# Optimization experiments

Measured on AMD Instinct MI355X. Metric: run time of the kernel, lower is better.

## Reference

```python
import jax, jax.numpy as jnp
import numpy as np

B, S, D, H = 2, 2048, 1024, 16
HD = D // H  # head_dim = 64
SCALE = HD ** -0.5


def setup_inputs() -> dict:
    key = jax.random.key(0)
    ks = jax.random.split(key, 5)
    s = 0.02
    return {
        "query": jax.random.normal(ks[0], (B, S, D), dtype=jnp.float32),
        "Wq": jax.random.normal(ks[1], (D, D), dtype=jnp.float32) * s,
        "bq": jnp.zeros((D,), dtype=jnp.float32),
        "Wk": jax.random.normal(ks[2], (D, D), dtype=jnp.float32) * s,
        "bk": jnp.zeros((D,), dtype=jnp.float32),
        "Wv": jax.random.normal(ks[3], (D, D), dtype=jnp.float32) * s,
        "bv": jnp.zeros((D,), dtype=jnp.float32),
        "Wo": jax.random.normal(ks[4], (D, D), dtype=jnp.float32) * s,
        "bo": jnp.zeros((D,), dtype=jnp.float32),
    }


def reference(query, Wq, bq, Wk, bk, Wv, bv, Wo, bo):
    b, s, _ = query.shape
    # QKV projections (self-attention: key = value = query)
    Q = (query @ Wq + bq).reshape(b, s, H, HD).transpose(0, 2, 1, 3)  # bhqd
    K = (query @ Wk + bk).reshape(b, s, H, HD).transpose(0, 2, 1, 3)  # bhkd
    V = (query @ Wv + bv).reshape(b, s, H, HD).transpose(0, 2, 1, 3)  # bhvd
    scores = jnp.einsum('bhqd,bhkd->bhqk', Q, K) * SCALE
    weights = jax.nn.softmax(scores, axis=-1)
    out = jnp.einsum('bhqk,bhkd->bhqd', weights, V)
    out = out.transpose(0, 2, 1, 3).reshape(b, s, D)
    return out @ Wo + bo
```

## Files before the change

kernel.cpp:

```cpp
#include <hip/hip_runtime.h>
#include <hip/hip_bf16.h>
#include <math.h>

#define B_ 2
#define S_ 2048
#define D_ 1024
#define H_ 16
#define HD_ 64
#define M_ (B_*S_)
#define C1_ 0.1803368798f

typedef float f32x4 __attribute__((ext_vector_type(4)));
typedef float f32x16 __attribute__((ext_vector_type(16)));
typedef short s16x8 __attribute__((ext_vector_type(8)));

__device__ __forceinline__ short f2bf(float f) {
  union { float f; unsigned u; } x; x.f = f;
  unsigned r = x.u + 0x7fffu + ((x.u >> 16) & 1u);
  return (short)(r >> 16);
}
__device__ __forceinline__ float bf2f(short v) {
  union { unsigned u; float f; } x; x.u = ((unsigned)(unsigned short)v) << 16;
  return x.f;
}
__device__ __forceinline__ unsigned cvt_pk_bf16(float a, float b) {
  unsigned r;
  asm("v_cvt_pk_bf16_f32 %0, %1, %2" : "=v"(r) : "v"(a), "v"(b));
  return r;
}
__device__ __forceinline__ float exp2_fast(float x) {
#if __has_builtin(__builtin_amdgcn_exp2f)
  return __builtin_amdgcn_exp2f(x);
#else
  float r; asm("v_exp_f32 %0, %1" : "=v"(r) : "v"(x)); return r;
#endif
}
__device__ __forceinline__ void gload_lds16(const void* g, void* l) {
  __builtin_amdgcn_global_load_lds(
      (const __attribute__((address_space(1))) void*)g,
      (__attribute__((address_space(3))) void*)l, 16, 0, 0);
}

__global__ __launch_bounds__(256) void k_prep(
    const float* __restrict__ query, short* __restrict__ xbf,
    const float* __restrict__ W0, const float* __restrict__ W1,
    const float* __restrict__ W2, const float* __restrict__ W3,
    short* __restrict__ T0, short* __restrict__ T1,
    short* __restrict__ T2, short* __restrict__ T3) {
  __shared__ short lt[64][72];
  const int blk = blockIdx.x;
  const int t = threadIdx.x;
  if (blk < 1024) {
    const int z = blk >> 8, tile = blk & 255;
    const float* W = z == 0 ? W0 : z == 1 ? W1 : z == 2 ? W2 : W3;
    short* Wt      = z == 0 ? T0 : z == 1 ? T1 : z == 2 ? T2 : T3;
    const int r0 = (tile >> 4) * 64;
    const int c0 = (tile & 15) * 64;
    const int rr = t >> 4, c4 = (t & 15) * 4;
    #pragma unroll
    for (int p = 0; p < 4; ++p) {
      int row = p * 16 + rr;
      f32x4 v = *reinterpret_cast<const f32x4*>(W + (size_t)(r0 + row) * D_ + c0 + c4);
      #pragma unroll
      for (int j = 0; j < 4; ++j) lt[c4 + j][row] = f2bf(v[j]);
    }
    __syncthreads();
    #pragma unroll
    for (int p = 0; p < 2; ++p) {
      int slot = p * 256 + t;
      int row = slot >> 3, s = slot & 7;
      s16x8 v = *reinterpret_cast<const s16x8*>(&lt[row][s * 8]);
      *reinterpret_cast<s16x8*>(Wt + (size_t)(c0 + row) * D_ + r0 + s * 8) = v;
    }
  } else {
    int i = ((blk - 1024) * 256 + t) * 8;
    f32x4 a = *reinterpret_cast<const f32x4*>(query + i);
    f32x4 b = *reinterpret_cast<const f32x4*>(query + i + 4);
    s16x8 v;
    v[0]=f2bf(a[0]); v[1]=f2bf(a[1]); v[2]=f2bf(a[2]); v[3]=f2bf(a[3]);
    v[4]=f2bf(b[0]); v[5]=f2bf(b[1]); v[6]=f2bf(b[2]); v[7]=f2bf(b[3]);
    *reinterpret_cast<s16x8*>(xbf + i) = v;
  }
}

__global__ __launch_bounds__(256) void k_gemm_qkv(
    const short* __restrict__ A,
    const short* __restrict__ WtQ, const short* __restrict__ WtK, const short* __restrict__ WtV,
    const float* __restrict__ bQ, const float* __restrict__ bK, const float* __restrict__ bV,
    short* __restrict__ Qo, short* __restrict__ Ko, short* __restrict__ Vto) {
  __shared__ __align__(16) char lds[65536];
  const int z = blockIdx.z;
  const short* Bt   = z == 0 ? WtQ : z == 1 ? WtK : WtV;
  const float* bias = z == 0 ? bQ  : z == 1 ? bK  : bV;
  const int t = threadIdx.x;
  const int lane = t & 63, wid = t >> 6;
  const int l15 = lane & 15, l4 = lane >> 4;
  const int wm = wid >> 1, wn = wid & 1;
  const int m0 = blockIdx.x * 128, n0 = blockIdx.y * 128;

  f32x4 acc[4][4];
  #pragma unroll
  for (int i = 0; i < 4; ++i)
    #pragma unroll
    for (int j = 0; j < 4; ++j) acc[i][j] = (f32x4){0.f, 0.f, 0.f, 0.f};

  auto stage = [&](int k0, int buf) {
    char* base = lds + buf * 32768;
    #pragma unroll
    for (int i = 0; i < 4; ++i) {
      int slot = t + i * 256;
      int row = slot >> 3, sw = (t & 7) ^ (row & 7);
      gload_lds16(A  + (size_t)(m0 + row) * D_ + k0 + sw * 8, base + (i * 256 + wid * 64) * 16);
      gload_lds16(Bt + (size_t)(n0 + row) * D_ + k0 + sw * 8, base + 16384 + (i * 256 + wid * 64) * 16);
    }
  };

  stage(0, 0);
  __syncthreads();

  int buf = 0;
  for (int k0 = 0; k0 < D_; k0 += 64, buf ^= 1) {
    if (k0 + 64 < D_) stage(k0 + 64, buf ^ 1);
    const char* bA = lds + buf * 32768;
    const char* bB = bA + 16384;
    #pragma unroll
    for (int ks = 0; ks < 2; ++ks) {
      s16x8 af[4], bf[4];
      #pragma unroll
      for (int mt = 0; mt < 4; ++mt) {
        int row = wm * 64 + mt * 16 + l15;
        af[mt] = *reinterpret_cast<const s16x8*>(bA + row * 128 + (((ks*4 + l4) ^ (row & 7)) * 16));
      }
      #pragma unroll
      for (int nt = 0; nt < 4; ++nt) {
        int row = wn * 64 + nt * 16 + l15;
        bf[nt] = *reinterpret_cast<const s16x8*>(bB + row * 128 + (((ks*4 + l4) ^ (row & 7)) * 16));
      }
      #pragma unroll
      for (int mt = 0; mt < 4; ++mt)
        #pragma unroll
        for (int nt = 0; nt < 4; ++nt)
          acc[mt][nt] = __builtin_amdgcn_mfma_f32_16x16x32_bf16(af[mt], bf[nt], acc[mt][nt], 0, 0, 0);
    }
    __syncthreads();
  }

  const float scale = (z == 0) ? C1_ : 1.f;
  #pragma unroll
  for (int nt = 0; nt < 4; ++nt) {
    int cl = wn * 64 + nt * 16 + l15;
    float bv = bias[n0 + cl];
    #pragma unroll
    for (int mt = 0; mt < 4; ++mt) {
      #pragma unroll
      for (int r = 0; r < 4; ++r) {
        int rl = wm * 64 + mt * 16 + l4 * 4 + r;
        short hv = f2bf((acc[mt][nt][r] + bv) * scale);
        if (z == 2) *reinterpret_cast<short*>(lds + cl * 256 + rl * 2) = hv;
        else        *reinterpret_cast<short*>(lds + rl * 256 + cl * 2) = hv;
      }
    }
  }
  __syncthreads();
  short* outp = (z == 0) ? Qo : (z == 1) ? Ko : Vto;
  const size_t ld   = (z == 2) ? (size_t)M_ : (size_t)D_;
  const int rowbase = (z == 2) ? n0 : m0;
  const int colbase = (z == 2) ? m0 : n0;
  #pragma unroll
  for (int p = 0; p < 8; ++p) {
    int slot = p * 256 + t;
    int row = slot >> 4, s = slot & 15;
    s16x8 v = *reinterpret_cast<const s16x8*>(lds + row * 256 + s * 16);
    *reinterpret_cast<s16x8*>(outp + (size_t)(rowbase + row) * ld + colbase + s * 8) = v;
  }
}

__global__ __launch_bounds__(256) void k_gemm_out(const short* __restrict__ A,
                                                  const short* __restrict__ Bt,
                                                  const float* __restrict__ bias,
                                                  float* __restrict__ C) {
  __shared__ __align__(16) char lds[49152];
  const int t = threadIdx.x;
  const int lane = t & 63, wid = t >> 6;
  const int l15 = lane & 15, l4 = lane >> 4;
  const int wm = wid >> 1, wn = wid & 1;
  const int m0 = blockIdx.x * 128, n0 = blockIdx.y * 64;

  f32x4 acc[4][2];
  #pragma unroll
  for (int i = 0; i < 4; ++i)
    #pragma unroll
    for (int j = 0; j < 2; ++j) acc[i][j] = (f32x4){0.f, 0.f, 0.f, 0.f};

  auto stage = [&](int k0, int buf) {
    char* base = lds + buf * 24576;
    #pragma unroll
    for (int i = 0; i < 4; ++i) {
      int slot = t + i * 256;
      int row = slot >> 3, sw = (t & 7) ^ (row & 7);
      gload_lds16(A + (size_t)(m0 + row) * D_ + k0 + sw * 8, base + (i * 256 + wid * 64) * 16);
    }
    #pragma unroll
    for (int i = 0; i < 2; ++i) {
      int slot = t + i * 256;
      int row = slot >> 3, sw = (t & 7) ^ (row & 7);
      gload_lds16(Bt + (size_t)(n0 + row) * D_ + k0 + sw * 8,
                  base + 16384 + (i * 256 + wid * 64) * 16);
    }
  };

  stage(0, 0);
  __syncthreads();

  int buf = 0;
  for (int k0 = 0; k0 < D_; k0 += 64, buf ^= 1) {
    if (k0 + 64 < D_) stage(k0 + 64, buf ^ 1);
    const char* bA = lds + buf * 24576;
    const char* bB = bA + 16384;
    #pragma unroll
    for (int ks = 0; ks < 2; ++ks) {
      s16x8 af[4], bf[2];
      #pragma unroll
      for (int mt = 0; mt < 4; ++mt) {
        int row = wm * 64 + mt * 16 + l15;
        af[mt] = *reinterpret_cast<const s16x8*>(bA + row * 128 + (((ks*4 + l4) ^ (row & 7)) * 16));
      }
      #pragma unroll
      for (int nt = 0; nt < 2; ++nt) {
        int row = wn * 32 + nt * 16 + l15;
        bf[nt] = *reinterpret_cast<const s16x8*>(bB + row * 128 + (((ks*4 + l4) ^ (row & 7)) * 16));
      }
      #pragma unroll
      for (int mt = 0; mt < 4; ++mt)
        #pragma unroll
        for (int nt = 0; nt < 2; ++nt)
          acc[mt][nt] = __builtin_amdgcn_mfma_f32_16x16x32_bf16(af[mt], bf[nt], acc[mt][nt], 0, 0, 0);
    }
    __syncthreads();
  }
  #pragma unroll
  for (int nt = 0; nt < 2; ++nt) {
    int col = n0 + wn * 32 + nt * 16 + l15;
    float bv = bias[col];
    #pragma unroll
    for (int mt = 0; mt < 4; ++mt) {
      int row0 = m0 + wm * 64 + mt * 16 + l4 * 4;
      #pragma unroll
      for (int r = 0; r < 4; ++r)
        C[(size_t)(row0 + r) * D_ + col] = acc[mt][nt][r] + bv;
    }
  }
}

__global__ __launch_bounds__(256, 4) void k_attn(const short* __restrict__ Q,
                                                 const short* __restrict__ K,
                                                 const short* __restrict__ Vt,
                                                 short* __restrict__ U0,
                                                 short* __restrict__ U1,
                                                 float* __restrict__ lsum) {
  __shared__ __align__(16) char lds[32768];
  const int t = threadIdx.x;
  const int lane = t & 63, wid = t >> 6;
  const int l31 = lane & 31, hi = lane >> 5;
  const int orig = blockIdx.x;
  const int xcd = orig & 7, idx = orig >> 3;
  const int bh = xcd * 4 + (idx >> 5);
  const int rem = idx & 31;
  const int qblk = rem >> 1;
  const int half = rem & 1;
  const int b = bh >> 4, h = bh & 15;
  const int q0 = qblk * 128;
  const size_t qkbase = (size_t)b * S_ * D_ + h * HD_;
  const short* gK = K + qkbase + (size_t)(half * (S_ / 2)) * D_;
  const short* gVt = Vt + (size_t)(h * HD_) * M_ + (size_t)b * S_ + half * (S_ / 2);
  short* Up = half ? U1 : U0;

  s16x8 qf[4];
  {
    const short* qp = Q + qkbase + (size_t)(q0 + wid * 32 + l31) * D_ + hi * 8;
    qf[0] = *reinterpret_cast<const s16x8*>(qp);
    qf[1] = *reinterpret_cast<const s16x8*>(qp + 16);
    qf[2] = *reinterpret_cast<const s16x8*>(qp + 32);
    qf[3] = *reinterpret_cast<const s16x8*>(qp + 48);
  }

  f32x16 oa[2];
  #pragma unroll
  for (int i = 0; i < 16; ++i) { oa[0][i] = 0.f; oa[1][i] = 0.f; }
  float l_run = 0.f;

  const int tr3 = t >> 3;
  const int ssw8 = ((t & 7) ^ (tr3 & 7)) * 8;
  const size_t kSrc = (size_t)tr3 * D_ + ssw8;
  const size_t vSrc = (size_t)tr3 * M_ + ssw8;

  const int s7 = l31 & 7;
  const int rbase = l31 * 128;
  int soff[4];
  #pragma unroll
  for (int ks = 0; ks < 4; ++ks) soff[ks] = ((2 * ks + hi) ^ s7) * 16;

  auto stage = [&](int tl, int bb) {
    if (tl >= S_ / 128) return;
    const short* pk = gK + (size_t)(tl * 64) * D_ + kSrc;
    const short* pv = gVt + tl * 64 + vSrc;
    char* dK = lds + bb * 8192 + wid * 1024;
    char* dV = dK + 16384;
    gload_lds16(pk, dK);
    gload_lds16(pk + (size_t)32 * D_, dK + 4096);
    gload_lds16(pv, dV);
    gload_lds16(pv + (size_t)32 * M_, dV + 4096);
  };

  auto tileFn = [&](int bb, int tl) {
    stage(tl + 1, bb ^ 1);
    const char* bK = lds + bb * 8192;
    const char* bV = bK + 16384;

    f32x16 sc[2];
    #pragma unroll
    for (int i = 0; i < 16; ++i) { sc[0][i] = 0.f; sc[1][i] = 0.f; }
    __builtin_amdgcn_s_setprio(1);
    #pragma unroll
    for (int ks = 0; ks < 4; ++ks)
      #pragma unroll
      for (int blk = 0; blk < 2; ++blk) {
        s16x8 kf = *reinterpret_cast<const s16x8*>(bK + blk * 4096 + rbase + soff[ks]);
        sc[blk] = __builtin_amdgcn_mfma_f32_32x32x16_bf16(kf, qf[ks], sc[blk], 0, 0, 0);
      }
    __builtin_amdgcn_s_setprio(0);

    float rs = 0.f;
    unsigned pkA[2][4], pkB[2][4];
    #pragma unroll
    for (int blk = 0; blk < 2; ++blk)
      #pragma unroll
      for (int g = 0; g < 4; ++g) {
        float p0 = exp2_fast(sc[blk][4*g+0]), p1 = exp2_fast(sc[blk][4*g+1]);
        float p2 = exp2_fast(sc[blk][4*g+2]), p3 = exp2_fast(sc[blk][4*g+3]);
        rs += (p0 + p1) + (p2 + p3);
        pkA[blk][g] = cvt_pk_bf16(p0, p1);
        pkB[blk][g] = cvt_pk_bf16(p2, p3);
      }
    rs += __shfl_xor(rs, 32);
    l_run += rs;

    __builtin_amdgcn_s_setprio(1);
    #pragma unroll
    for (int sp = 0; sp < 4; ++sp) {
      const int blk = sp >> 1, su = sp & 1;
      unsigned a0 = pkA[blk][2*su],     a1 = pkB[blk][2*su];
      unsigned b0 = pkA[blk][2*su + 1], b1 = pkB[blk][2*su + 1];
      asm("v_permlane32_swap_b32 %0, %1" : "+v"(a0), "+v"(b0));
      asm("v_permlane32_swap_b32 %0, %1" : "+v"(a1), "+v"(b1));
      union { unsigned u[4]; s16x8 v; } pw;
      pw.u[0] = a0; pw.u[1] = a1; pw.u[2] = b0; pw.u[3] = b1;
      #pragma unroll
      for (int dblk = 0; dblk < 2; ++dblk) {
        s16x8 vf = *reinterpret_cast<const s16x8*>(bV + dblk * 4096 + rbase + soff[sp]);
        oa[dblk] = __builtin_amdgcn_mfma_f32_32x32x16_bf16(pw.v, vf, oa[dblk], 0, 0, 0);
      }
    }
    __builtin_amdgcn_s_setprio(0);
    __syncthreads();
  };

  stage(0, 0);
  __syncthreads();
  #pragma unroll 1
  for (int it = 0; it < S_ / 256; ++it) {
    tileFn(0, 2 * it);
    tileFn(1, 2 * it + 1);
  }

  char* myl = lds + wid * 4096;
  #pragma unroll
  for (int reg = 0; reg < 16; ++reg) {
    int qrow = (reg & 3) + 8 * (reg >> 2) + 4 * hi;
    *reinterpret_cast<short*>(myl + qrow * 128 + l31 * 2)        = f2bf(oa[0][reg]);
    *reinterpret_cast<short*>(myl + qrow * 128 + (32 + l31) * 2) = f2bf(oa[1][reg]);
  }
  #pragma unroll
  for (int i = 0; i < 4; ++i) {
    int slot = i * 64 + lane;
    int row = slot >> 3, s = slot & 7;
    s16x8 v = *reinterpret_cast<const s16x8*>(myl + slot * 16);
    *reinterpret_cast<s16x8*>(
        Up + qkbase + (size_t)(q0 + wid * 32 + row) * D_ + s * 8) = v;
  }
  if (hi == 0)
    lsum[((half * 32 + bh) << 11) + q0 + wid * 32 + l31] = l_run;
}

__global__ __launch_bounds__(256) void k_merge(const short* U0, const short* U1,
                                               const float* lsum, short* out) {
  int i = (blockIdx.x * 256 + threadIdx.x) * 8;
  int row = i >> 10;
  int col = i & 1023;
  int b = row >> 11, s = row & 2047;
  int bh = b * 16 + (col >> 6);
  float l0 = lsum[(bh << 11) + s];
  float l1 = lsum[((32 + bh) << 11) + s];
  float inv = 1.f / (l0 + l1);
  s16x8 u0 = *reinterpret_cast<const s16x8*>(U0 + i);
  s16x8 u1 = *reinterpret_cast<const s16x8*>(U1 + i);
  s16x8 r;
  #pragma unroll
  for (int j = 0; j < 8; ++j) r[j] = f2bf((bf2f(u0[j]) + bf2f(u1[j])) * inv);
  *reinterpret_cast<s16x8*>(out + i) = r;
}

extern "C" void kernel_launch(void* const* d_in, const int* in_sizes, int n_in,
                              void* d_out, int out_size, void* d_ws, size_t ws_size,
                              hipStream_t stream) {
  const float* query = (const float*)d_in[0];
  const float* Wq = (const float*)d_in[1];
  const float* bq = (const float*)d_in[2];
  const float* Wk = (const float*)d_in[3];
  const float* bk = (const float*)d_in[4];
  const float* Wv = (const float*)d_in[5];
  const float* bv = (const float*)d_in[6];
  const float* Wo = (const float*)d_in[7];
  const float* bo = (const float*)d_in[8];
  float* out = (float*)d_out;

  const size_t NE = (size_t)M_ * D_;
  short* ws   = (short*)d_ws;
  short* xbf  = ws;
  short* qbf  = ws + NE;
  short* kbf  = ws + 2 * NE;
  short* vtbf = ws + 3 * NE;
  short* aout = ws + 4 * NE;
  short* wtq  = ws + 5 * NE;
  short* wtk  = wtq + (size_t)D_ * D_;
  short* wtv  = wtk + (size_t)D_ * D_;
  short* wto  = wtv + (size_t)D_ * D_;

  short* U0 = aout;
  short* U1 = xbf;
  float* lsb = (float*)wtq;

  k_prep<<<3072, 256, 0, stream>>>(query, xbf, Wq, Wk, Wv, Wo, wtq, wtk, wtv, wto);

  k_gemm_qkv<<<dim3(M_ / 128, D_ / 128, 3), 256, 0, stream>>>(
      xbf, wtq, wtk, wtv, bq, bk, bv, qbf, kbf, vtbf);

  k_attn<<<1024, 256, 0, stream>>>(qbf, kbf, vtbf, U0, U1, lsb);
  k_merge<<<(int)(NE / (8 * 256)), 256, 0, stream>>>(U0, U1, lsb, aout);

  k_gemm_out<<<dim3(M_ / 128, D_ / 64), 256, 0, stream>>>(aout, wto, bo, out);
}
```

Baseline: 102.2 us.

## Process two 32-row query tiles per wave in attention to reuse K/V fragments

Each wave now handles 64 query rows, split into two 32-row sub-tiles, instead of 32. Every K and V fragment read from LDS feeds two MFMAs, which halves LDS traffic and global K/V staging per query row. The grid is halved to 512 blocks and launch bounds drop to 2 blocks per SIMD to make room for the doubled accumulators and Q fragments. The cost is higher register pressure and lower occupancy, so there are fewer waves to hide latency.

```diff
diff --git a/kernel.cpp b/kernel.cpp
--- a/kernel.cpp
+++ b/kernel.cpp
@@ -252,7 +252,7 @@
   }
 }
 
-__global__ __launch_bounds__(256, 4) void k_attn(const short* __restrict__ Q,
+__global__ __launch_bounds__(256, 2) void k_attn(const short* __restrict__ Q,
                                                  const short* __restrict__ K,
                                                  const short* __restrict__ Vt,
                                                  short* __restrict__ U0,
@@ -264,30 +264,32 @@
   const int l31 = lane & 31, hi = lane >> 5;
   const int orig = blockIdx.x;
   const int xcd = orig & 7, idx = orig >> 3;
-  const int bh = xcd * 4 + (idx >> 5);
-  const int rem = idx & 31;
+  const int bh = xcd * 4 + (idx >> 4);
+  const int rem = idx & 15;
   const int qblk = rem >> 1;
   const int half = rem & 1;
   const int b = bh >> 4, h = bh & 15;
-  const int q0 = qblk * 128;
+  const int q0 = qblk * 256;
   const size_t qkbase = (size_t)b * S_ * D_ + h * HD_;
   const short* gK = K + qkbase + (size_t)(half * (S_ / 2)) * D_;
   const short* gVt = Vt + (size_t)(h * HD_) * M_ + (size_t)b * S_ + half * (S_ / 2);
   short* Up = half ? U1 : U0;
 
-  s16x8 qf[4];
+  s16x8 qfA[4], qfB[4];
   {
-    const short* qp = Q + qkbase + (size_t)(q0 + wid * 32 + l31) * D_ + hi * 8;
-    qf[0] = *reinterpret_cast<const s16x8*>(qp);
-    qf[1] = *reinterpret_cast<const s16x8*>(qp + 16);
-    qf[2] = *reinterpret_cast<const s16x8*>(qp + 32);
-    qf[3] = *reinterpret_cast<const s16x8*>(qp + 48);
-  }
-
-  f32x16 oa[2];
-  #pragma unroll
-  for (int i = 0; i < 16; ++i) { oa[0][i] = 0.f; oa[1][i] = 0.f; }
-  float l_run = 0.f;
+    const short* qa = Q + qkbase + (size_t)(q0 + wid * 64 + l31) * D_ + hi * 8;
+    const short* qb = qa + (size_t)32 * D_;
+    #pragma unroll
+    for (int ks = 0; ks < 4; ++ks) {
+      qfA[ks] = *reinterpret_cast<const s16x8*>(qa + ks * 16);
+      qfB[ks] = *reinterpret_cast<const s16x8*>(qb + ks * 16);
+    }
+  }
+
+  f32x16 oaA[2], oaB[2];
+  #pragma unroll
+  for (int i = 0; i < 16; ++i) { oaA[0][i] = 0.f; oaA[1][i] = 0.f; oaB[0][i] = 0.f; oaB[1][i] = 0.f; }
+  float lA = 0.f, lB = 0.f;
 
   const int tr3 = t >> 3;
   const int ssw8 = ((t & 7) ^ (tr3 & 7)) * 8;
@@ -317,48 +319,63 @@
     const char* bK = lds + bb * 8192;
     const char* bV = bK + 16384;
 
-    f32x16 sc[2];
-    #pragma unroll
-    for (int i = 0; i < 16; ++i) { sc[0][i] = 0.f; sc[1][i] = 0.f; }
+    f32x16 scA[2], scB[2];
+    #pragma unroll
+    for (int i = 0; i < 16; ++i) { scA[0][i] = 0.f; scA[1][i] = 0.f; scB[0][i] = 0.f; scB[1][i] = 0.f; }
     __builtin_amdgcn_s_setprio(1);
     #pragma unroll
     for (int ks = 0; ks < 4; ++ks)
       #pragma unroll
       for (int blk = 0; blk < 2; ++blk) {
         s16x8 kf = *reinterpret_cast<const s16x8*>(bK + blk * 4096 + rbase + soff[ks]);
-        sc[blk] = __builtin_amdgcn_mfma_f32_32x32x16_bf16(kf, qf[ks], sc[blk], 0, 0, 0);
+        scA[blk] = __builtin_amdgcn_mfma_f32_32x32x16_bf16(kf, qfA[ks], scA[blk], 0, 0, 0);
+        scB[blk] = __builtin_amdgcn_mfma_f32_32x32x16_bf16(kf, qfB[ks], scB[blk], 0, 0, 0);
       }
     __builtin_amdgcn_s_setprio(0);
 
-    float rs = 0.f;
-    unsigned pkA[2][4], pkB[2][4];
+    float rsA = 0.f, rsB = 0.f;
+    unsigned pA1[2][4], pA2[2][4], pB1[2][4], pB2[2][4];
     #pragma unroll
     for (int blk = 0; blk < 2; ++blk)
       #pragma unroll
       for (int g = 0; g < 4; ++g) {
-        float p0 = exp2_fast(sc[blk][4*g+0]), p1 = exp2_fast(sc[blk][4*g+1]);
-        float p2 = exp2_fast(sc[blk][4*g+2]), p3 = exp2_fast(sc[blk][4*g+3]);
-        rs += (p0 + p1) + (p2 + p3);
-        pkA[blk][g] = cvt_pk_bf16(p0, p1);
-        pkB[blk][g] = cvt_pk_bf16(p2, p3);
-      }
-    rs += __shfl_xor(rs, 32);
-    l_run += rs;
+        float a0 = exp2_fast(scA[blk][4*g+0]), a1 = exp2_fast(scA[blk][4*g+1]);
+        float a2 = exp2_fast(scA[blk][4*g+2]), a3 = exp2_fast(scA[blk][4*g+3]);
+        rsA += (a0 + a1) + (a2 + a3);
+        pA1[blk][g] = cvt_pk_bf16(a0, a1);
+        pA2[blk][g] = cvt_pk_bf16(a2, a3);
+        float b0 = exp2_fast(scB[blk][4*g+0]), b1 = exp2_fast(scB[blk][4*g+1]);
+        float b2 = exp2_fast(scB[blk][4*g+2]), b3 = exp2_fast(scB[blk][4*g+3]);
+        rsB += (b0 + b1) + (b2 + b3);
+        pB1[blk][g] = cvt_pk_bf16(b0, b1);
+        pB2[blk][g] = cvt_pk_bf16(b2, b3);
+      }
+    rsA += __shfl_xor(rsA, 32);
+    rsB += __shfl_xor(rsB, 32);
+    lA += rsA;
+    lB += rsB;
 
     __builtin_amdgcn_s_setprio(1);
     #pragma unroll
     for (int sp = 0; sp < 4; ++sp) {
       const int blk = sp >> 1, su = sp & 1;
-      unsigned a0 = pkA[blk][2*su],     a1 = pkB[blk][2*su];
-      unsigned b0 = pkA[blk][2*su + 1], b1 = pkB[blk][2*su + 1];
-      asm("v_permlane32_swap_b32 %0, %1" : "+v"(a0), "+v"(b0));
-      asm("v_permlane32_swap_b32 %0, %1" : "+v"(a1), "+v"(b1));
-      union { unsigned u[4]; s16x8 v; } pw;
-      pw.u[0] = a0; pw.u[1] = a1; pw.u[2] = b0; pw.u[3] = b1;
+      unsigned xa0 = pA1[blk][2*su],     xa1 = pA2[blk][2*su];
+      unsigned xb0 = pA1[blk][2*su + 1], xb1 = pA2[blk][2*su + 1];
+      asm("v_permlane32_swap_b32 %0, %1" : "+v"(xa0), "+v"(xb0));
+      asm("v_permlane32_swap_b32 %0, %1" : "+v"(xa1), "+v"(xb1));
+      union { unsigned u[4]; s16x8 v; } pwA;
+      pwA.u[0] = xa0; pwA.u[1] = xa1; pwA.u[2] = xb0; pwA.u[3] = xb1;
+      unsigned ya0 = pB1[blk][2*su],     ya1 = pB2[blk][2*su];
+      unsigned yb0 = pB1[blk][2*su + 1], yb1 = pB2[blk][2*su + 1];
+      asm("v_permlane32_swap_b32 %0, %1" : "+v"(ya0), "+v"(yb0));
+      asm("v_permlane32_swap_b32 %0, %1" : "+v"(ya1), "+v"(yb1));
+      union { unsigned u[4]; s16x8 v; } pwB;
+      pwB.u[0] = ya0; pwB.u[1] = ya1; pwB.u[2] = yb0; pwB.u[3] = yb1;
       #pragma unroll
       for (int dblk = 0; dblk < 2; ++dblk) {
         s16x8 vf = *reinterpret_cast<const s16x8*>(bV + dblk * 4096 + rbase + soff[sp]);
-        oa[dblk] = __builtin_amdgcn_mfma_f32_32x32x16_bf16(pw.v, vf, oa[dblk], 0, 0, 0);
+        oaA[dblk] = __builtin_amdgcn_mfma_f32_32x32x16_bf16(pwA.v, vf, oaA[dblk], 0, 0, 0);
+        oaB[dblk] = __builtin_amdgcn_mfma_f32_32x32x16_bf16(pwB.v, vf, oaB[dblk], 0, 0, 0);
       }
     }
     __builtin_amdgcn_s_setprio(0);
@@ -373,23 +390,28 @@
     tileFn(1, 2 * it + 1);
   }
 
-  char* myl = lds + wid * 4096;
+  char* myl = lds + wid * 8192;
   #pragma unroll
   for (int reg = 0; reg < 16; ++reg) {
     int qrow = (reg & 3) + 8 * (reg >> 2) + 4 * hi;
-    *reinterpret_cast<short*>(myl + qrow * 128 + l31 * 2)        = f2bf(oa[0][reg]);
-    *reinterpret_cast<short*>(myl + qrow * 128 + (32 + l31) * 2) = f2bf(oa[1][reg]);
-  }
-  #pragma unroll
-  for (int i = 0; i < 4; ++i) {
+    *reinterpret_cast<short*>(myl + qrow * 128 + l31 * 2)              = f2bf(oaA[0][reg]);
+    *reinterpret_cast<short*>(myl + qrow * 128 + (32 + l31) * 2)       = f2bf(oaA[1][reg]);
+    *reinterpret_cast<short*>(myl + (32 + qrow) * 128 + l31 * 2)       = f2bf(oaB[0][reg]);
+    *reinterpret_cast<short*>(myl + (32 + qrow) * 128 + (32 + l31) * 2) = f2bf(oaB[1][reg]);
+  }
+  #pragma unroll
+  for (int i = 0; i < 8; ++i) {
     int slot = i * 64 + lane;
     int row = slot >> 3, s = slot & 7;
     s16x8 v = *reinterpret_cast<const s16x8*>(myl + slot * 16);
     *reinterpret_cast<s16x8*>(
-        Up + qkbase + (size_t)(q0 + wid * 32 + row) * D_ + s * 8) = v;
-  }
-  if (hi == 0)
-    lsum[((half * 32 + bh) << 11) + q0 + wid * 32 + l31] = l_run;
+        Up + qkbase + (size_t)(q0 + wid * 64 + row) * D_ + s * 8) = v;
+  }
+  if (hi == 0) {
+    int qb = ((half * 32 + bh) << 11) + q0 + wid * 64 + l31;
+    lsum[qb] = lA;
+    lsum[qb + 32] = lB;
+  }
 }
 
 __global__ __launch_bounds__(256) void k_merge(const short* U0, const short* U1,
@@ -445,7 +467,7 @@
   k_gemm_qkv<<<dim3(M_ / 128, D_ / 128, 3), 256, 0, stream>>>(
       xbf, wtq, wtk, wtv, bq, bk, bv, qbf, kbf, vtbf);
 
-  k_attn<<<1024, 256, 0, stream>>>(qbf, kbf, vtbf, U0, U1, lsb);
+  k_attn<<<512, 256, 0, stream>>>(qbf, kbf, vtbf, U0, U1, lsb);
   k_merge<<<(int)(NE / (8 * 256)), 256, 0, stream>>>(U0, U1, lsb, aout);
 
   k_gemm_out<<<dim3(M_ / 128, D_ / 64), 256, 0, stream>>>(aout, wto, bo, out);
```

New measurement: 100.6 us (median of 2 runs). About the same (-1.6%).

## Software-pipeline QK with softmax/PV and split KV four ways in attention

Applied to the files above, without the earlier changes.

Restructures the attention kernel so the QK^T MFMAs for the next key tile are issued before the softmax and PV work of the current tile. K gets four LDS buffers and V gets two, growing LDS to 48 KB, and launch bounds drop from 4 to 2 blocks per CU. It also templates the key-split count and, when the workspace is large enough, splits keys four ways over twice as many blocks, with a merge kernel that sums four partial outputs. The aim is better overlap of matrix and exp work and more parallelism, at the cost of lower occupancy and extra partial-output memory traffic in the merge.

```diff
diff --git a/kernel.cpp b/kernel.cpp
--- a/kernel.cpp
+++ b/kernel.cpp
@@ -252,42 +252,45 @@
   }
 }
 
-__global__ __launch_bounds__(256, 4) void k_attn(const short* __restrict__ Q,
+template <int NSPLIT>
+__global__ __launch_bounds__(256, 2) void k_attn(const short* __restrict__ Q,
                                                  const short* __restrict__ K,
                                                  const short* __restrict__ Vt,
-                                                 short* __restrict__ U0,
-                                                 short* __restrict__ U1,
+                                                 short* __restrict__ UA,
+                                                 short* __restrict__ UB,
+                                                 short* __restrict__ UC,
+                                                 short* __restrict__ UD,
                                                  float* __restrict__ lsum) {
-  __shared__ __align__(16) char lds[32768];
+  __shared__ __align__(16) char lds[49152];
   const int t = threadIdx.x;
   const int lane = t & 63, wid = t >> 6;
   const int l31 = lane & 31, hi = lane >> 5;
   const int orig = blockIdx.x;
   const int xcd = orig & 7, idx = orig >> 3;
-  const int bh = xcd * 4 + (idx >> 5);
-  const int rem = idx & 31;
-  const int qblk = rem >> 1;
-  const int half = rem & 1;
+  const int bh = xcd * 4 + idx / (16 * NSPLIT);
+  const int rem = idx % (16 * NSPLIT);
+  const int qblk = rem / NSPLIT;
+  const int split = rem % NSPLIT;
   const int b = bh >> 4, h = bh & 15;
   const int q0 = qblk * 128;
   const size_t qkbase = (size_t)b * S_ * D_ + h * HD_;
-  const short* gK = K + qkbase + (size_t)(half * (S_ / 2)) * D_;
-  const short* gVt = Vt + (size_t)(h * HD_) * M_ + (size_t)b * S_ + half * (S_ / 2);
-  short* Up = half ? U1 : U0;
+  const short* gK = K + qkbase + (size_t)(split * (S_ / NSPLIT)) * D_;
+  const short* gVt = Vt + (size_t)(h * HD_) * M_ + (size_t)b * S_ + split * (S_ / NSPLIT);
+  short* Up = (split == 0) ? UA : (split == 1) ? UB : (split == 2) ? UC : UD;
+  const int TILES = (S_ / 64) / NSPLIT;
 
   s16x8 qf[4];
   {
     const short* qp = Q + qkbase + (size_t)(q0 + wid * 32 + l31) * D_ + hi * 8;
-    qf[0] = *reinterpret_cast<const s16x8*>(qp);
-    qf[1] = *reinterpret_cast<const s16x8*>(qp + 16);
-    qf[2] = *reinterpret_cast<const s16x8*>(qp + 32);
-    qf[3] = *reinterpret_cast<const s16x8*>(qp + 48);
+    #pragma unroll
+    for (int ks = 0; ks < 4; ++ks)
+      qf[ks] = *reinterpret_cast<const s16x8*>(qp + ks * 16);
   }
 
   f32x16 oa[2];
   #pragma unroll
   for (int i = 0; i < 16; ++i) { oa[0][i] = 0.f; oa[1][i] = 0.f; }
-  float l_run = 0.f;
+  float lAcc = 0.f;
 
   const int tr3 = t >> 3;
   const int ssw8 = ((t & 7) ^ (tr3 & 7)) * 8;
@@ -300,77 +303,93 @@
   #pragma unroll
   for (int ks = 0; ks < 4; ++ks) soff[ks] = ((2 * ks + hi) ^ s7) * 16;
 
-  auto stage = [&](int tl, int bb) {
-    if (tl >= S_ / 128) return;
+  auto stage_K = [&](int tl, int kb) {
+    if (tl >= TILES) return;
     const short* pk = gK + (size_t)(tl * 64) * D_ + kSrc;
-    const short* pv = gVt + tl * 64 + vSrc;
-    char* dK = lds + bb * 8192 + wid * 1024;
-    char* dV = dK + 16384;
+    char* dK = lds + kb * 8192 + wid * 1024;
     gload_lds16(pk, dK);
     gload_lds16(pk + (size_t)32 * D_, dK + 4096);
+  };
+  auto stage_V = [&](int tl, int vb) {
+    if (tl >= TILES) return;
+    const short* pv = gVt + tl * 64 + vSrc;
+    char* dV = lds + 32768 + vb * 8192 + wid * 1024;
     gload_lds16(pv, dV);
     gload_lds16(pv + (size_t)32 * M_, dV + 4096);
   };
 
-  auto tileFn = [&](int bb, int tl) {
-    stage(tl + 1, bb ^ 1);
-    const char* bK = lds + bb * 8192;
-    const char* bV = bK + 16384;
-
-    f32x16 sc[2];
-    #pragma unroll
-    for (int i = 0; i < 16; ++i) { sc[0][i] = 0.f; sc[1][i] = 0.f; }
+  auto qk_step = [&](int kb, f32x16* sc) {
     __builtin_amdgcn_s_setprio(1);
     #pragma unroll
     for (int ks = 0; ks < 4; ++ks)
       #pragma unroll
       for (int blk = 0; blk < 2; ++blk) {
-        s16x8 kf = *reinterpret_cast<const s16x8*>(bK + blk * 4096 + rbase + soff[ks]);
+        s16x8 kf = *reinterpret_cast<const s16x8*>(lds + kb * 8192 + blk * 4096 + rbase + soff[ks]);
         sc[blk] = __builtin_amdgcn_mfma_f32_32x32x16_bf16(kf, qf[ks], sc[blk], 0, 0, 0);
       }
     __builtin_amdgcn_s_setprio(0);
-
+  };
+
+  auto sm_pv = [&](f32x16* sc, int vb) {
     float rs = 0.f;
-    unsigned pkA[2][4], pkB[2][4];
+    unsigned p1[2][4], p2[2][4];
     #pragma unroll
     for (int blk = 0; blk < 2; ++blk)
       #pragma unroll
       for (int g = 0; g < 4; ++g) {
-        float p0 = exp2_fast(sc[blk][4*g+0]), p1 = exp2_fast(sc[blk][4*g+1]);
-        float p2 = exp2_fast(sc[blk][4*g+2]), p3 = exp2_fast(sc[blk][4*g+3]);
-        rs += (p0 + p1) + (p2 + p3);
-        pkA[blk][g] = cvt_pk_bf16(p0, p1);
-        pkB[blk][g] = cvt_pk_bf16(p2, p3);
+        float a0 = exp2_fast(sc[blk][4*g+0]), a1 = exp2_fast(sc[blk][4*g+1]);
+        float a2 = exp2_fast(sc[blk][4*g+2]), a3 = exp2_fast(sc[blk][4*g+3]);
+        rs += (a0 + a1) + (a2 + a3);
+        p1[blk][g] = cvt_pk_bf16(a0, a1);
+        p2[blk][g] = cvt_pk_bf16(a2, a3);
       }
     rs += __shfl_xor(rs, 32);
-    l_run += rs;
-
+    lAcc += rs;
     __builtin_amdgcn_s_setprio(1);
     #pragma unroll
     for (int sp = 0; sp < 4; ++sp) {
       const int blk = sp >> 1, su = sp & 1;
-      unsigned a0 = pkA[blk][2*su],     a1 = pkB[blk][2*su];
-      unsigned b0 = pkA[blk][2*su + 1], b1 = pkB[blk][2*su + 1];
-      asm("v_permlane32_swap_b32 %0, %1" : "+v"(a0), "+v"(b0));
-      asm("v_permlane32_swap_b32 %0, %1" : "+v"(a1), "+v"(b1));
+      unsigned x0 = p1[blk][2*su],     x1 = p2[blk][2*su];
+      unsigned y0 = p1[blk][2*su + 1], y1 = p2[blk][2*su + 1];
+      asm("v_permlane32_swap_b32 %0, %1" : "+v"(x0), "+v"(y0));
+      asm("v_permlane32_swap_b32 %0, %1" : "+v"(x1), "+v"(y1));
       union { unsigned u[4]; s16x8 v; } pw;
-      pw.u[0] = a0; pw.u[1] = a1; pw.u[2] = b0; pw.u[3] = b1;
+      pw.u[0] = x0; pw.u[1] = x1; pw.u[2] = y0; pw.u[3] = y1;
       #pragma unroll
       for (int dblk = 0; dblk < 2; ++dblk) {
-        s16x8 vf = *reinterpret_cast<const s16x8*>(bV + dblk * 4096 + rbase + soff[sp]);
+        s16x8 vf = *reinterpret_cast<const s16x8*>(
+            lds + 32768 + vb * 8192 + dblk * 4096 + rbase + soff[sp]);
         oa[dblk] = __builtin_amdgcn_mfma_f32_32x32x16_bf16(pw.v, vf, oa[dblk], 0, 0, 0);
       }
     }
     __builtin_amdgcn_s_setprio(0);
+  };
+
+  stage_K(0, 0);
+  stage_V(0, 0);
+  stage_K(1, 1);
+  __syncthreads();
+  f32x16 scA[2], scB[2];
+  #pragma unroll
+  for (int i = 0; i < 16; ++i) { scA[0][i] = 0.f; scA[1][i] = 0.f; }
+  qk_step(0, scA);
+
+  #pragma unroll 1
+  for (int it = 0; it < TILES; it += 2) {
+    #pragma unroll
+    for (int i = 0; i < 16; ++i) { scB[0][i] = 0.f; scB[1][i] = 0.f; }
+    if (it + 1 < TILES) qk_step((it + 1) & 3, scB);
+    stage_K(it + 2, (it + 2) & 3);
+    stage_V(it + 1, (it + 1) & 1);
+    sm_pv(scA, it & 1);
     __syncthreads();
-  };
-
-  stage(0, 0);
-  __syncthreads();
-  #pragma unroll 1
-  for (int it = 0; it < S_ / 256; ++it) {
-    tileFn(0, 2 * it);
-    tileFn(1, 2 * it + 1);
+    #pragma unroll
+    for (int i = 0; i < 16; ++i) { scA[0][i] = 0.f; scA[1][i] = 0.f; }
+    if (it + 2 < TILES) qk_step((it + 2) & 3, scA);
+    stage_K(it + 3, (it + 3) & 3);
+    stage_V(it + 2, (it + 2) & 1);
+    sm_pv(scB, (it + 1) & 1);
+    __syncthreads();
   }
 
   char* myl = lds + wid * 4096;
@@ -389,24 +408,36 @@
         Up + qkbase + (size_t)(q0 + wid * 32 + row) * D_ + s * 8) = v;
   }
   if (hi == 0)
-    lsum[((half * 32 + bh) << 11) + q0 + wid * 32 + l31] = l_run;
-}
-
+    lsum[((split * 32 + bh) << 11) + q0 + wid * 32 + l31] = lAcc;
+}
+
+template <int NSPLIT>
 __global__ __launch_bounds__(256) void k_merge(const short* U0, const short* U1,
+                                               const short* U2, const short* U3,
                                                const float* lsum, short* out) {
   int i = (blockIdx.x * 256 + threadIdx.x) * 8;
   int row = i >> 10;
   int col = i & 1023;
   int b = row >> 11, s = row & 2047;
   int bh = b * 16 + (col >> 6);
-  float l0 = lsum[(bh << 11) + s];
-  float l1 = lsum[((32 + bh) << 11) + s];
-  float inv = 1.f / (l0 + l1);
+  float lt = 0.f;
+  #pragma unroll
+  for (int sp = 0; sp < NSPLIT; ++sp) lt += lsum[((sp * 32 + bh) << 11) + s];
+  float inv = 1.f / lt;
+  float acc[8];
   s16x8 u0 = *reinterpret_cast<const s16x8*>(U0 + i);
   s16x8 u1 = *reinterpret_cast<const s16x8*>(U1 + i);
+  #pragma unroll
+  for (int j = 0; j < 8; ++j) acc[j] = bf2f(u0[j]) + bf2f(u1[j]);
+  if (NSPLIT == 4) {
+    s16x8 u2 = *reinterpret_cast<const s16x8*>(U2 + i);
+    s16x8 u3 = *reinterpret_cast<const s16x8*>(U3 + i);
+    #pragma unroll
+    for (int j = 0; j < 8; ++j) acc[j] += bf2f(u2[j]) + bf2f(u3[j]);
+  }
   s16x8 r;
   #pragma unroll
-  for (int j = 0; j < 8; ++j) r[j] = f2bf((bf2f(u0[j]) + bf2f(u1[j])) * inv);
+  for (int j = 0; j < 8; ++j) r[j] = f2bf(acc[j] * inv);
   *reinterpret_cast<s16x8*>(out + i) = r;
 }
 
@@ -435,18 +466,27 @@
   short* wtk  = wtq + (size_t)D_ * D_;
   short* wtv  = wtk + (size_t)D_ * D_;
   short* wto  = wtv + (size_t)D_ * D_;
+  short* U2   = ws + 6 * NE;
+  short* U3   = ws + 7 * NE;
 
   short* U0 = aout;
   short* U1 = xbf;
   float* lsb = (float*)wtq;
 
+  const bool split4 = ws_size >= (size_t)8 * NE * sizeof(short);
+
   k_prep<<<3072, 256, 0, stream>>>(query, xbf, Wq, Wk, Wv, Wo, wtq, wtk, wtv, wto);
 
   k_gemm_qkv<<<dim3(M_ / 128, D_ / 128, 3), 256, 0, stream>>>(
       xbf, wtq, wtk, wtv, bq, bk, bv, qbf, kbf, vtbf);
 
-  k_attn<<<1024, 256, 0, stream>>>(qbf, kbf, vtbf, U0, U1, lsb);
-  k_merge<<<(int)(NE / (8 * 256)), 256, 0, stream>>>(U0, U1, lsb, aout);
+  if (split4) {
+    k_attn<4><<<2048, 256, 0, stream>>>(qbf, kbf, vtbf, U0, U1, U2, U3, lsb);
+    k_merge<4><<<(int)(NE / (8 * 256)), 256, 0, stream>>>(U0, U1, U2, U3, lsb, aout);
+  } else {
+    k_attn<2><<<1024, 256, 0, stream>>>(qbf, kbf, vtbf, U0, U1, U0, U1, lsb);
+    k_merge<2><<<(int)(NE / (8 * 256)), 256, 0, stream>>>(U0, U1, U0, U1, lsb, aout);
+  }
 
   k_gemm_out<<<dim3(M_ / 128, D_ / 64), 256, 0, stream>>>(aout, wto, bo, out);
 }
```

Measured after the change: 110.5 us. 8.1% more time.
